# Performance work log

Measured on AMD Instinct MI355X. Metric: run time of the kernel, lower is better.

The kernel has to match this reference:

```python
import jax, jax.numpy as jnp
import numpy as np

B, S, DIM = 2, 2048, 1024
H, DH = 16, 64
WIN = 512


def setup_inputs() -> dict:
    key = jax.random.key(0)
    k1, k2, k3 = jax.random.split(key, 3)
    x = jax.random.normal(k1, (B, S, DIM), dtype=jnp.float32)
    Wqkv = jax.random.normal(k2, (DIM, 3 * H * DH), dtype=jnp.float32) * (DIM ** -0.5)
    Wout = jax.random.normal(k3, (H * DH, DIM), dtype=jnp.float32) * ((H * DH) ** -0.5)
    return {"x": x, "Wqkv": Wqkv, "Wout": Wout}


def reference(x, Wqkv, Wout):
    b, s, _ = x.shape
    qkv = jnp.einsum('bsd,de->bse', x, Wqkv)  # (B,S,3*H*DH)
    q, k, v = jnp.split(qkv, 3, axis=-1)
    # -> (B,H,S,DH)
    q = q.reshape(b, s, H, DH).transpose(0, 2, 1, 3)
    k = k.reshape(b, s, H, DH).transpose(0, 2, 1, 3)
    v = v.reshape(b, s, H, DH).transpose(0, 2, 1, 3)
    scale = DH ** -0.5  # attention sees per-head dim
    scores = jnp.einsum('bhsd,bhtd->bhst', q, k) * scale  # dense (B,H,S,S)
    i = jnp.arange(s)[:, None]
    j = jnp.arange(s)[None, :]
    mask = (j >= i - WIN + 1) & (j <= i)  # causal sliding window
    mask_value = -jnp.finfo(scores.dtype).max
    scores = jnp.where(mask[None, None], scores, mask_value)
    attn = jax.nn.softmax(scores, axis=-1)
    out = jnp.einsum('bhst,bhtd->bhsd', attn, v)
    out = out.transpose(0, 2, 1, 3).reshape(b, s, H * DH)
    return jnp.einsum('bse,ed->bsd', out, Wout)
```

## Files before the change

### kernel.cpp

```cpp
#include <hip/hip_runtime.h>

#define S_LEN 2048
#define BATCH 2
#define HDIM 1024
#define NH 16
#define DH 64
#define WINSZ 512
#define MROWS (BATCH * S_LEN)

typedef __attribute__((ext_vector_type(8))) short bfrag;
typedef __attribute__((ext_vector_type(4))) float f32x4;
typedef __attribute__((ext_vector_type(4))) int i128;

__device__ __forceinline__ short f2bf(float f) {
    union { float f; unsigned u; } v;
    v.f = f;
    unsigned r = v.u + 0x7fffu + ((v.u >> 16) & 1u);
    return (short)(r >> 16);
}

__device__ __forceinline__ void gload_lds16(const short* g, short* l) {
    __builtin_amdgcn_global_load_lds(
        (const __attribute__((address_space(1))) unsigned int*)g,
        (__attribute__((address_space(3))) unsigned int*)l, 16, 0, 0);
}

__global__ void cast_bf_kernel(const float* __restrict__ in, short* __restrict__ out, int n4) {
    int i = blockIdx.x * blockDim.x + threadIdx.x;
    if (i < n4) {
        float4 v = ((const float4*)in)[i];
        union { short s[4]; int2 p; } u;
        u.s[0] = f2bf(v.x); u.s[1] = f2bf(v.y); u.s[2] = f2bf(v.z); u.s[3] = f2bf(v.w);
        ((int2*)out)[i] = u.p;
    }
}

__global__ void transpose_cast_kernel(const float* __restrict__ in, short* __restrict__ out,
                                      int R, int C) {
    __shared__ float tile[32][33];
    int tc0 = blockIdx.x * 32;
    int tr0 = blockIdx.y * 32;
    int t = threadIdx.x;
    int c = t & 31, r0 = t >> 5;
    #pragma unroll
    for (int k = 0; k < 4; ++k) {
        int r = r0 + k * 8;
        tile[r][c] = in[(size_t)(tr0 + r) * C + tc0 + c];
    }
    __syncthreads();
    int r2 = t & 31, c0 = t >> 5;
    #pragma unroll
    for (int k = 0; k < 4; ++k) {
        int c2 = c0 + k * 8;
        out[(size_t)(tc0 + c2) * R + tr0 + r2] = f2bf(tile[r2][c2]);
    }
}

__global__ __launch_bounds__(256, 2)
void gemm_bt(const short* __restrict__ A, const short* __restrict__ Bt,
             int M, int N, int K, int mode,
             short* __restrict__ qo, short* __restrict__ ko, short* __restrict__ vto,
             float* __restrict__ co)
{
    __shared__ __align__(16) short Al[128 * 32];
    __shared__ __align__(16) short Bl[128 * 32];
    const int t = threadIdx.x;
    const int lane = t & 63;
    const int wave = t >> 6;
    const int wr = wave >> 1, wc = wave & 1;
    const int m0 = blockIdx.y * 128, n0 = blockIdx.x * 128;
    const int lrow = lane & 15;
    const int lk8 = (lane >> 4) << 3;

    f32x4 acc[4][4];
    #pragma unroll
    for (int m = 0; m < 4; ++m)
        #pragma unroll
        for (int n = 0; n < 4; ++n)
            acc[m][n] = (f32x4){0.f, 0.f, 0.f, 0.f};

    const int ci0 = t;
    const int row0s = ci0 >> 2, col0s = (ci0 & 3) << 3;
    const int ci1 = 256 + t;
    const int row1s = ci1 >> 2, col1s = (ci1 & 3) << 3;
    short* AlB0 = &Al[(size_t)(wave * 64) * 8];
    short* BlB0 = &Bl[(size_t)(wave * 64) * 8];
    short* AlB1 = &Al[(size_t)(256 + wave * 64) * 8];
    short* BlB1 = &Bl[(size_t)(256 + wave * 64) * 8];

    for (int k0 = 0; k0 < K; k0 += 32) {
        gload_lds16(&A[(size_t)(m0 + row0s) * K + k0 + col0s], AlB0);
        gload_lds16(&Bt[(size_t)(n0 + row0s) * K + k0 + col0s], BlB0);
        gload_lds16(&A[(size_t)(m0 + row1s) * K + k0 + col1s], AlB1);
        gload_lds16(&Bt[(size_t)(n0 + row1s) * K + k0 + col1s], BlB1);
        __syncthreads();
        bfrag af[4], bfr[4];
        #pragma unroll
        for (int m = 0; m < 4; ++m)
            af[m] = *(const bfrag*)(&Al[(wr * 64 + m * 16 + lrow) * 32 + lk8]);
        #pragma unroll
        for (int n = 0; n < 4; ++n)
            bfr[n] = *(const bfrag*)(&Bl[(wc * 64 + n * 16 + lrow) * 32 + lk8]);
        #pragma unroll
        for (int m = 0; m < 4; ++m)
            #pragma unroll
            for (int n = 0; n < 4; ++n)
                acc[m][n] = __builtin_amdgcn_mfma_f32_16x16x32_bf16(af[m], bfr[n], acc[m][n], 0, 0, 0);
        __syncthreads();
    }

    if (mode == 1) {
        #pragma unroll
        for (int m = 0; m < 4; ++m) {
            #pragma unroll
            for (int n = 0; n < 4; ++n) {
                int col = n0 + wc * 64 + n * 16 + lrow;
                int row0 = m0 + wr * 64 + m * 16 + ((lane >> 4) << 2);
                #pragma unroll
                for (int r = 0; r < 4; ++r)
                    co[(size_t)(row0 + r) * N + col] = acc[m][n][r];
            }
        }
    } else {
        #pragma unroll
        for (int m = 0; m < 4; ++m) {
            #pragma unroll
            for (int n = 0; n < 4; ++n) {
                int col = n0 + wc * 64 + n * 16 + lrow;
                int which = col >> 10;
                int rem = col & 1023;
                int h = rem >> 6, dh = rem & 63;
                int row0 = m0 + wr * 64 + m * 16 + ((lane >> 4) << 2);
                #pragma unroll
                for (int r = 0; r < 4; ++r) {
                    int row = row0 + r;
                    int b = row >> 11, s = row & 2047;
                    short val = f2bf(acc[m][n][r]);
                    if (which == 0)
                        qo[(((size_t)(b * NH + h)) * S_LEN + s) * DH + dh] = val;
                    else if (which == 1)
                        ko[(((size_t)(b * NH + h)) * S_LEN + s) * DH + dh] = val;
                    else
                        vto[(((size_t)(b * NH + h)) * DH + dh) * S_LEN + s] = val;
                }
            }
        }
    }
}

__global__ __launch_bounds__(256, 4)
void attn_kernel(const short* __restrict__ q_bf, const short* __restrict__ k_bf,
                 const short* __restrict__ vt, short* __restrict__ attno)
{
    __shared__ __align__(16) short Kl[2][64 * 64];
    __shared__ __align__(16) short Vl[2][64 * 64];
    __shared__ __align__(16) short Pl[4][16 * 64];

    const int bid = blockIdx.x;
    const int logical = (bid & 7) * 128 + (bid >> 3);
    const int qblk = logical & 31;
    const int bh = logical >> 5;

    const int t = threadIdx.x;
    const int wave = t >> 6, lane = t & 63;
    const int qb0 = qblk * 64;
    const int i0 = qb0 + wave * 16;
    const short* qp = q_bf + (size_t)bh * S_LEN * DH;
    const short* kp = k_bf + (size_t)bh * S_LEN * DH;
    const short* vp = vt + (size_t)bh * DH * S_LEN;
    char* myP = (char*)&Pl[wave][0];

    const int lq = lane & 15;
    const int g = lane >> 4;
    const int swz = (lq & 7) << 4;
    const int l7 = lq & 7;

    bfrag qf[2];
    qf[0] = *(const bfrag*)(&qp[(i0 + lq) * DH + (g << 3)]);
    qf[1] = *(const bfrag*)(&qp[(i0 + lq) * DH + 32 + (g << 3)]);

    f32x4 oacc[4];
    #pragma unroll
    for (int d = 0; d < 4; ++d) oacc[d] = (f32x4){0.f, 0.f, 0.f, 0.f};
    float m2 = -1e30f, lrun = 0.f;
    const float QSCALE = 0.125f * 1.44269504f;
    const int qi = i0 + lq;

    int j_lo = qb0 - (WINSZ - 1);
    if (j_lo < 0) j_lo = 0;
    j_lo &= ~63;
    const int nT = ((qb0 + 64) - j_lo) >> 6;

    auto stage = [&](int j0, short* kbuf, short* vbuf) {
        #pragma unroll
        for (int qq = 0; qq < 2; ++qq) {
            int chunk = qq * 256 + wave * 64 + lane;
            int row = chunk >> 3;
            int cc = (chunk & 7) ^ (row & 7);
            short* kdst = kbuf + (size_t)(qq * 256 + wave * 64) * 8;
            short* vdst = vbuf + (size_t)(qq * 256 + wave * 64) * 8;
            gload_lds16(kp + (size_t)(j_lo + j0 + row) * DH + cc * 8, kdst);
            gload_lds16(vp + (size_t)row * S_LEN + j_lo + j0 + cc * 8, vdst);
        }
    };

    stage(0, Kl[0], Vl[0]);
    __syncthreads();

    for (int ti = 0; ti < nT; ++ti) {
        const int cur = ti & 1;
        const int j0 = j_lo + ti * 64;
        if (ti + 1 < nT) stage((ti + 1) * 64, Kl[cur ^ 1], Vl[cur ^ 1]);

        const short* Kc = Kl[cur];
        const short* Vc = Vl[cur];

        f32x4 sc[4];
        #pragma unroll
        for (int tc = 0; tc < 4; ++tc) {
            bfrag a0 = *(const bfrag*)(&Kc[(tc * 16 + lq) * 64 + ((g ^ l7) << 3)]);
            bfrag a1 = *(const bfrag*)(&Kc[(tc * 16 + lq) * 64 + (((4 | g) ^ l7) << 3)]);
            f32x4 z = (f32x4){0.f, 0.f, 0.f, 0.f};
            z = __builtin_amdgcn_mfma_f32_16x16x32_bf16(a0, qf[0], z, 0, 0, 0);
            z = __builtin_amdgcn_mfma_f32_16x16x32_bf16(a1, qf[1], z, 0, 0, 0);
            sc[tc] = z;
        }

        const bool nomask = (j0 >= i0 - (WINSZ - 16)) && (j0 + 63 <= i0);
        float s[4][4];
        float pm = -1e30f;
        #pragma unroll
        for (int tc = 0; tc < 4; ++tc) {
            #pragma unroll
            for (int r = 0; r < 4; ++r) {
                float sv = sc[tc][r] * QSCALE;
                if (!nomask) {
                    int kj = j0 + tc * 16 + 4 * g + r;
                    sv = ((kj <= qi) && (kj > qi - WINSZ)) ? sv : -1e30f;
                }
                s[tc][r] = sv;
                pm = fmaxf(pm, sv);
            }
        }
        pm = fmaxf(pm, __shfl_xor(pm, 16));
        pm = fmaxf(pm, __shfl_xor(pm, 32));
        float mnew = fmaxf(m2, pm);
        float scale_old = exp2f(m2 - mnew);
        m2 = mnew;
        float p[4][4];
        float rs = 0.f;
        #pragma unroll
        for (int tc = 0; tc < 4; ++tc)
            #pragma unroll
            for (int r = 0; r < 4; ++r) {
                p[tc][r] = exp2f(s[tc][r] - mnew);
                rs += p[tc][r];
            }
        rs += __shfl_xor(rs, 16);
        rs += __shfl_xor(rs, 32);
        lrun = lrun * scale_old + rs;
        #pragma unroll
        for (int d = 0; d < 4; ++d) {
            f32x4 o = oacc[d];
            o[0] *= scale_old; o[1] *= scale_old; o[2] *= scale_old; o[3] *= scale_old;
            oacc[d] = o;
        }

        #pragma unroll
        for (int tc = 0; tc < 4; ++tc) {
            union { short sh[4]; int2 w; } u;
            u.sh[0] = f2bf(p[tc][0]); u.sh[1] = f2bf(p[tc][1]);
            u.sh[2] = f2bf(p[tc][2]); u.sh[3] = f2bf(p[tc][3]);
            int wb = (lq * 128 + tc * 32 + g * 8) ^ swz;
            *(int2*)(myP + wb) = u.w;
        }
        asm volatile("s_waitcnt lgkmcnt(0)" ::: "memory");

        #pragma unroll
        for (int kt = 0; kt < 2; ++kt) {
            int rb = (lq * 128 + kt * 64 + g * 16) ^ swz;
            bfrag pf = *(const bfrag*)(myP + rb);
            #pragma unroll
            for (int d = 0; d < 4; ++d) {
                bfrag vfr = *(const bfrag*)(&Vc[(d * 16 + lq) * 64 + (((kt * 4 + g) ^ l7) << 3)]);
                oacc[d] = __builtin_amdgcn_mfma_f32_16x16x32_bf16(vfr, pf, oacc[d], 0, 0, 0);
            }
        }
        __syncthreads();
    }

    const int b = bh >> 4, h = bh & 15;
    const float inv_l = 1.f / lrun;
    size_t rowbase = ((size_t)(b * S_LEN + qi)) * HDIM + h * DH;
    #pragma unroll
    for (int d = 0; d < 4; ++d) {
        union { short sh[4]; int2 w; } u;
        #pragma unroll
        for (int r = 0; r < 4; ++r)
            u.sh[r] = f2bf(oacc[d][r] * inv_l);
        *(int2*)(&attno[rowbase + d * 16 + 4 * g]) = u.w;
    }
}

extern "C" void kernel_launch(void* const* d_in, const int* in_sizes, int n_in,
                              void* d_out, int out_size, void* d_ws, size_t ws_size,
                              hipStream_t stream) {
    const float* x = (const float*)d_in[0];
    const float* Wqkv = (const float*)d_in[1];
    const float* Wout = (const float*)d_in[2];
    float* out = (float*)d_out;
    char* ws = (char*)d_ws;

    short* x_bf   = (short*)(ws);
    short* wqkv_t = (short*)(ws + 8388608);
    short* wout_t = (short*)(ws + 14680064);
    short* q_bf   = (short*)(ws + 16777216);
    short* k_bf   = (short*)(ws + 25165824);
    short* v_t    = (short*)(ws + 33554432);
    short* attno  = (short*)(ws + 41943040);

    cast_bf_kernel<<<4096, 256, 0, stream>>>(x, x_bf, MROWS * HDIM / 4);
    transpose_cast_kernel<<<dim3(96, 32), 256, 0, stream>>>(Wqkv, wqkv_t, 1024, 3072);
    transpose_cast_kernel<<<dim3(32, 32), 256, 0, stream>>>(Wout, wout_t, 1024, 1024);

    gemm_bt<<<dim3(24, 32), 256, 0, stream>>>(x_bf, wqkv_t, MROWS, 3 * HDIM, HDIM, 0,
                                              q_bf, k_bf, v_t, nullptr);
    attn_kernel<<<dim3(BATCH * NH * (S_LEN / 64)), 256, 0, stream>>>(q_bf, k_bf, v_t, attno);
    gemm_bt<<<dim3(8, 32), 256, 0, stream>>>(attno, wout_t, MROWS, HDIM, HDIM, 1,
                                             nullptr, nullptr, nullptr, out);
}
```

Before: 175.9 us.

## Double-buffer GEMM LDS staging and write QKV row-major with separate V transpose

New measurement: 175.0 us. No clear change (-0.5%).

```diff
diff --git a/kernel.cpp b/kernel.cpp
--- a/kernel.cpp
+++ b/kernel.cpp
@@ -59,11 +59,10 @@
 __global__ __launch_bounds__(256, 2)
 void gemm_bt(const short* __restrict__ A, const short* __restrict__ Bt,
              int M, int N, int K, int mode,
-             short* __restrict__ qo, short* __restrict__ ko, short* __restrict__ vto,
-             float* __restrict__ co)
+             short* __restrict__ cbf, float* __restrict__ co)
 {
-    __shared__ __align__(16) short Al[128 * 32];
-    __shared__ __align__(16) short Bl[128 * 32];
+    __shared__ __align__(16) short Al[2][128 * 32];
+    __shared__ __align__(16) short Bl[2][128 * 32];
     const int t = threadIdx.x;
     const int lane = t & 63;
     const int wave = t >> 6;
@@ -79,28 +78,31 @@
         for (int n = 0; n < 4; ++n)
             acc[m][n] = (f32x4){0.f, 0.f, 0.f, 0.f};
 
-    const int ci0 = t;
-    const int row0s = ci0 >> 2, col0s = (ci0 & 3) << 3;
-    const int ci1 = 256 + t;
-    const int row1s = ci1 >> 2, col1s = (ci1 & 3) << 3;
-    short* AlB0 = &Al[(size_t)(wave * 64) * 8];
-    short* BlB0 = &Bl[(size_t)(wave * 64) * 8];
-    short* AlB1 = &Al[(size_t)(256 + wave * 64) * 8];
-    short* BlB1 = &Bl[(size_t)(256 + wave * 64) * 8];
-
-    for (int k0 = 0; k0 < K; k0 += 32) {
-        gload_lds16(&A[(size_t)(m0 + row0s) * K + k0 + col0s], AlB0);
-        gload_lds16(&Bt[(size_t)(n0 + row0s) * K + k0 + col0s], BlB0);
-        gload_lds16(&A[(size_t)(m0 + row1s) * K + k0 + col1s], AlB1);
-        gload_lds16(&Bt[(size_t)(n0 + row1s) * K + k0 + col1s], BlB1);
-        __syncthreads();
+    const int row0s = t >> 2, col0s = (t & 3) << 3;
+    const int row1s = (256 + t) >> 2, col1s = (t & 3) << 3;
+    const size_t dst0 = (size_t)(wave * 64) * 8;
+    const size_t dst1 = (size_t)(256 + wave * 64) * 8;
+
+    auto stage = [&](int k0, int sb) {
+        gload_lds16(&A[(size_t)(m0 + row0s) * K + k0 + col0s], &Al[sb][0] + dst0);
+        gload_lds16(&Bt[(size_t)(n0 + row0s) * K + k0 + col0s], &Bl[sb][0] + dst0);
+        gload_lds16(&A[(size_t)(m0 + row1s) * K + k0 + col1s], &Al[sb][0] + dst1);
+        gload_lds16(&Bt[(size_t)(n0 + row1s) * K + k0 + col1s], &Bl[sb][0] + dst1);
+    };
+
+    const int nk = K >> 5;
+    stage(0, 0);
+    __syncthreads();
+    for (int ki = 0; ki < nk; ++ki) {
+        const int cur = ki & 1;
+        if (ki + 1 < nk) stage((ki + 1) << 5, cur ^ 1);
         bfrag af[4], bfr[4];
         #pragma unroll
         for (int m = 0; m < 4; ++m)
-            af[m] = *(const bfrag*)(&Al[(wr * 64 + m * 16 + lrow) * 32 + lk8]);
+            af[m] = *(const bfrag*)(&Al[cur][(wr * 64 + m * 16 + lrow) * 32 + lk8]);
         #pragma unroll
         for (int n = 0; n < 4; ++n)
-            bfr[n] = *(const bfrag*)(&Bl[(wc * 64 + n * 16 + lrow) * 32 + lk8]);
+            bfr[n] = *(const bfrag*)(&Bl[cur][(wc * 64 + n * 16 + lrow) * 32 + lk8]);
         #pragma unroll
         for (int m = 0; m < 4; ++m)
             #pragma unroll
@@ -111,7 +113,7 @@
 
     if (mode == 1) {
         #pragma unroll
-        for (int m = 0; m < 4; ++m) {
+        for (int m = 0; m < 4; ++m)
             #pragma unroll
             for (int n = 0; n < 4; ++n) {
                 int col = n0 + wc * 64 + n * 16 + lrow;
@@ -120,37 +122,44 @@
                 for (int r = 0; r < 4; ++r)
                     co[(size_t)(row0 + r) * N + col] = acc[m][n][r];
             }
-        }
     } else {
         #pragma unroll
-        for (int m = 0; m < 4; ++m) {
+        for (int m = 0; m < 4; ++m)
             #pragma unroll
             for (int n = 0; n < 4; ++n) {
                 int col = n0 + wc * 64 + n * 16 + lrow;
-                int which = col >> 10;
-                int rem = col & 1023;
-                int h = rem >> 6, dh = rem & 63;
                 int row0 = m0 + wr * 64 + m * 16 + ((lane >> 4) << 2);
                 #pragma unroll
-                for (int r = 0; r < 4; ++r) {
-                    int row = row0 + r;
-                    int b = row >> 11, s = row & 2047;
-                    short val = f2bf(acc[m][n][r]);
-                    if (which == 0)
-                        qo[(((size_t)(b * NH + h)) * S_LEN + s) * DH + dh] = val;
-                    else if (which == 1)
-                        ko[(((size_t)(b * NH + h)) * S_LEN + s) * DH + dh] = val;
-                    else
-                        vto[(((size_t)(b * NH + h)) * DH + dh) * S_LEN + s] = val;
-                }
-            }
-        }
-    }
+                for (int r = 0; r < 4; ++r)
+                    cbf[(size_t)(row0 + r) * N + col] = f2bf(acc[m][n][r]);
+            }
+    }
+}
+
+__global__ __launch_bounds__(256)
+void vtr_kernel(const short* __restrict__ qkv, short* __restrict__ vt) {
+    __shared__ __align__(16) short tile[64][72];
+    const int bh = blockIdx.x >> 5;
+    const int s0 = (blockIdx.x & 31) << 6;
+    const int b = bh >> 4, h = bh & 15;
+    const short* src = qkv + (size_t)b * S_LEN * 3072 + 2048 + h * 64;
+    const int t = threadIdx.x;
+    const int sl = t >> 2, dh0 = (t & 3) << 4;
+    *(i128*)&tile[sl][dh0]     = *(const i128*)&src[(size_t)(s0 + sl) * 3072 + dh0];
+    *(i128*)&tile[sl][dh0 + 8] = *(const i128*)&src[(size_t)(s0 + sl) * 3072 + dh0 + 8];
+    __syncthreads();
+    const int dhl = t >> 2, sc = (t & 3) << 4;
+    union { short sh[8]; i128 v; } u0, u1;
+    #pragma unroll
+    for (int i = 0; i < 8; ++i) { u0.sh[i] = tile[sc + i][dhl]; u1.sh[i] = tile[sc + 8 + i][dhl]; }
+    short* dst = vt + ((size_t)bh * DH + dhl) * S_LEN + s0 + sc;
+    *(i128*)&dst[0] = u0.v;
+    *(i128*)&dst[8] = u1.v;
 }
 
 __global__ __launch_bounds__(256, 4)
-void attn_kernel(const short* __restrict__ q_bf, const short* __restrict__ k_bf,
-                 const short* __restrict__ vt, short* __restrict__ attno)
+void attn_kernel(const short* __restrict__ qkv, const short* __restrict__ vt,
+                 short* __restrict__ attno)
 {
     __shared__ __align__(16) short Kl[2][64 * 64];
     __shared__ __align__(16) short Vl[2][64 * 64];
@@ -160,13 +169,14 @@
     const int logical = (bid & 7) * 128 + (bid >> 3);
     const int qblk = logical & 31;
     const int bh = logical >> 5;
+    const int b = bh >> 4, h = bh & 15;
 
     const int t = threadIdx.x;
     const int wave = t >> 6, lane = t & 63;
     const int qb0 = qblk * 64;
     const int i0 = qb0 + wave * 16;
-    const short* qp = q_bf + (size_t)bh * S_LEN * DH;
-    const short* kp = k_bf + (size_t)bh * S_LEN * DH;
+    const short* qbase = qkv + (size_t)b * S_LEN * 3072 + h * 64;
+    const short* kbase = qkv + (size_t)b * S_LEN * 3072 + 1024 + h * 64;
     const short* vp = vt + (size_t)bh * DH * S_LEN;
     char* myP = (char*)&Pl[wave][0];
 
@@ -176,8 +186,8 @@
     const int l7 = lq & 7;
 
     bfrag qf[2];
-    qf[0] = *(const bfrag*)(&qp[(i0 + lq) * DH + (g << 3)]);
-    qf[1] = *(const bfrag*)(&qp[(i0 + lq) * DH + 32 + (g << 3)]);
+    qf[0] = *(const bfrag*)(&qbase[(size_t)(i0 + lq) * 3072 + (g << 3)]);
+    qf[1] = *(const bfrag*)(&qbase[(size_t)(i0 + lq) * 3072 + 32 + (g << 3)]);
 
     f32x4 oacc[4];
     #pragma unroll
@@ -199,7 +209,7 @@
             int cc = (chunk & 7) ^ (row & 7);
             short* kdst = kbuf + (size_t)(qq * 256 + wave * 64) * 8;
             short* vdst = vbuf + (size_t)(qq * 256 + wave * 64) * 8;
-            gload_lds16(kp + (size_t)(j_lo + j0 + row) * DH + cc * 8, kdst);
+            gload_lds16(kbase + (size_t)(j_lo + j0 + row) * 3072 + cc * 8, kdst);
             gload_lds16(vp + (size_t)row * S_LEN + j_lo + j0 + cc * 8, vdst);
         }
     };
@@ -230,7 +240,7 @@
         float s[4][4];
         float pm = -1e30f;
         #pragma unroll
-        for (int tc = 0; tc < 4; ++tc) {
+        for (int tc = 0; tc < 4; ++tc)
             #pragma unroll
             for (int r = 0; r < 4; ++r) {
                 float sv = sc[tc][r] * QSCALE;
@@ -241,7 +251,6 @@
                 s[tc][r] = sv;
                 pm = fmaxf(pm, sv);
             }
-        }
         pm = fmaxf(pm, __shfl_xor(pm, 16));
         pm = fmaxf(pm, __shfl_xor(pm, 32));
         float mnew = fmaxf(m2, pm);
@@ -289,7 +298,6 @@
         __syncthreads();
     }
 
-    const int b = bh >> 4, h = bh & 15;
     const float inv_l = 1.f / lrun;
     size_t rowbase = ((size_t)(b * S_LEN + qi)) * HDIM + h * DH;
     #pragma unroll
@@ -314,18 +322,18 @@
     short* x_bf   = (short*)(ws);
     short* wqkv_t = (short*)(ws + 8388608);
     short* wout_t = (short*)(ws + 14680064);
-    short* q_bf   = (short*)(ws + 16777216);
-    short* k_bf   = (short*)(ws + 25165824);
-    short* v_t    = (short*)(ws + 33554432);
-    short* attno  = (short*)(ws + 41943040);
+    short* qkv_rm = (short*)(ws + 16777216);
+    short* v_t    = (short*)(ws + 41943040);
+    short* attno  = x_bf;
 
     cast_bf_kernel<<<4096, 256, 0, stream>>>(x, x_bf, MROWS * HDIM / 4);
     transpose_cast_kernel<<<dim3(96, 32), 256, 0, stream>>>(Wqkv, wqkv_t, 1024, 3072);
     transpose_cast_kernel<<<dim3(32, 32), 256, 0, stream>>>(Wout, wout_t, 1024, 1024);
 
     gemm_bt<<<dim3(24, 32), 256, 0, stream>>>(x_bf, wqkv_t, MROWS, 3 * HDIM, HDIM, 0,
-                                              q_bf, k_bf, v_t, nullptr);
-    attn_kernel<<<dim3(BATCH * NH * (S_LEN / 64)), 256, 0, stream>>>(q_bf, k_bf, v_t, attno);
+                                              qkv_rm, nullptr);
+    vtr_kernel<<<1024, 256, 0, stream>>>(qkv_rm, v_t);
+    attn_kernel<<<dim3(BATCH * NH * (S_LEN / 64)), 256, 0, stream>>>(qkv_rm, v_t, attno);
     gemm_bt<<<dim3(8, 32), 256, 0, stream>>>(attno, wout_t, MROWS, HDIM, HDIM, 1,
-                                             nullptr, nullptr, nullptr, out);
-}
+                                             nullptr, out);
+}
```
